# Kernel tuning notes

Measured on AMD Instinct MI355X. Metric: run time of the kernel, lower is better.

## Reference

```python
import jax, jax.numpy as jnp
import numpy as np

B, S, D, DQKV = 4, 2048, 1024, 1024

def setup_inputs() -> dict:
    key = jax.random.key(0)
    kx, kq, kk, kv = jax.random.split(key, 4)
    scale = 1.0 / np.sqrt(D)
    return {
        "x": jax.random.normal(kx, (B, S, D), dtype=jnp.float32),
        "wq": jax.random.normal(kq, (D, DQKV), dtype=jnp.float32) * scale,
        "wk": jax.random.normal(kk, (D, DQKV), dtype=jnp.float32) * scale,
        "wv": jax.random.normal(kv, (D, DQKV), dtype=jnp.float32) * scale,
    }

def reference(x, wq, wk, wv):
    # QKV projections: [B,S,D] @ [D,Dqkv] -> [B,S,Dqkv]
    q = jnp.einsum('bsd,de->bse', x, wq)
    k = jnp.einsum('bsd,de->bse', x, wk)
    v = jnp.einsum('bsd,de->bse', x, wv)
    # scores: [B,S,S], scaled by sqrt(dim_qkv)
    scores = jnp.einsum('bik,bjk->bij', q, k) / jnp.sqrt(jnp.asarray(DQKV, dtype=x.dtype))
    attn = jax.nn.softmax(scores, axis=-1)
    # output: [B,S,Dqkv]
    return jnp.einsum('bij,bjd->bid', attn, v)
```

## Files before the change

### kernel.cpp

```cpp
#include <hip/hip_runtime.h>
#include <cstdint>
#include <cstddef>

typedef __bf16 bf16;
typedef __bf16 bf16x4 __attribute__((ext_vector_type(4)));
typedef __bf16 bf16x8 __attribute__((ext_vector_type(8)));
typedef float  f32x4  __attribute__((ext_vector_type(4)));

#define BATCH 4
#define SEQ   2048
#define DIM   1024

__device__ __forceinline__ bf16 to_bf16(float f) {
    unsigned u = __builtin_bit_cast(unsigned, f);
    u += 0x7fffu + ((u >> 16) & 1u);
    unsigned short h = (unsigned short)(u >> 16);
    return __builtin_bit_cast(bf16, h);
}

__device__ __forceinline__ void load16_lds(const bf16* g, bf16* l) {
    __builtin_amdgcn_global_load_lds(
        (__attribute__((address_space(1))) void*)(g),
        (__attribute__((address_space(3))) void*)(l),
        16, 0, 0);
}

__device__ __forceinline__ void gemm_core64(
    const bf16* __restrict__ Abase, const bf16* __restrict__ Bbase,
    int K, int lda, int ldb, bf16* As, bf16* Bs, f32x4 acc[4][4])
{
    const int tid  = threadIdx.x;
    const int lane = tid & 63;
    const int wave = tid >> 6;
    const int wm   = (wave >> 1) * 64;
    const int wn   = (wave & 1) * 64;
    const int r16  = lane & 15;
    const int g    = lane >> 4;
    const int srow0 = wave * 8 + (lane >> 3);
    const int scoff = (((lane & 7) ^ ((lane >> 3) & 7)) * 8);
    const int ldsW  = wave * 512;

    for (int k0 = 0; k0 < K; k0 += 64) {
        __syncthreads();
#pragma unroll
        for (int j = 0; j < 4; ++j) {
            load16_lds(Abase + (size_t)(j * 32 + srow0) * lda + k0 + scoff,
                       As + j * 2048 + ldsW);
            load16_lds(Bbase + (size_t)(j * 32 + srow0) * ldb + k0 + scoff,
                       Bs + j * 2048 + ldsW);
        }
        __syncthreads();

#pragma unroll
        for (int h = 0; h < 2; ++h) {
            bf16x8 af[4], bfr[4];
            const int pc = h * 4 + g;
#pragma unroll
            for (int i = 0; i < 4; ++i) {
                const int p = pc ^ (r16 & 7);
                af[i]  = *(const bf16x8*)(As + (wm + i * 16 + r16) * 64 + p * 8);
                bfr[i] = *(const bf16x8*)(Bs + (wn + i * 16 + r16) * 64 + p * 8);
            }
#pragma unroll
            for (int mi = 0; mi < 4; ++mi)
#pragma unroll
                for (int ni = 0; ni < 4; ++ni)
                    acc[mi][ni] = __builtin_amdgcn_mfma_f32_16x16x32_bf16(
                        af[mi], bfr[ni], acc[mi][ni], 0, 0, 0);
        }
    }
}

__global__ __launch_bounds__(256, 4) void proj_gemm(
    const bf16* __restrict__ xb, const bf16* __restrict__ Wt,
    bf16* __restrict__ QK, bf16* __restrict__ Vt)
{
    __shared__ bf16 As[8192];
    __shared__ bf16 Bs[8192];
    f32x4 acc[4][4] = {};

    const int r = blockIdx.x;
    const bf16 *Ab, *Bb;
    bf16* Cb;
    int bx, byl;
    if (r < 1024) {
        const int c = r & 7, j = r >> 3;
        bx  = j & 15;
        byl = c + 8 * (j >> 4);
        Ab = xb + (size_t)byl * 128 * DIM;
        Bb = Wt + (size_t)bx * 128 * DIM;
        Cb = QK + (size_t)byl * 128 * 2048;
    } else {
        const int u = r - 1024;
        const int c = u & 7, j = u >> 3;
        bx = j & 15;
        const int p = c + 8 * (j >> 4);
        byl = p & 7;
        const int bz = p >> 3;
        Ab = Wt + (size_t)2 * DIM * DIM + (size_t)byl * 128 * DIM;
        Bb = xb + (size_t)bz * SEQ * DIM + (size_t)bx * 128 * DIM;
        Cb = Vt + (size_t)bz * DIM * SEQ + (size_t)byl * 128 * 2048;
    }
    gemm_core64(Ab, Bb, DIM, DIM, DIM, As, Bs, acc);

    const int lane = threadIdx.x & 63;
    const int wave = threadIdx.x >> 6;
    const int wm = (wave >> 1) * 64, wn = (wave & 1) * 64;
    const int rowO = wm + ((lane >> 4) * 4);
    const int colO = bx * 128 + wn + (lane & 15);
#pragma unroll
    for (int mi = 0; mi < 4; ++mi)
#pragma unroll
        for (int ni = 0; ni < 4; ++ni)
#pragma unroll
            for (int rr = 0; rr < 4; ++rr)
                Cb[(size_t)(rowO + mi * 16 + rr) * 2048 + colO + ni * 16] =
                    to_bf16(acc[mi][ni][rr]);
}

__global__ __launch_bounds__(256, 4) void gemm_scores(
    const bf16* __restrict__ A, const bf16* __restrict__ Bm, bf16* __restrict__ C,
    float* __restrict__ lsum)
{
    __shared__ bf16 As[8192];
    __shared__ bf16 Bs[8192];
    f32x4 acc[4][4] = {};

    const int d = blockIdx.x + 16 * (blockIdx.y + 16 * blockIdx.z);
    const int c = d & 7, j = d >> 3;
    const int bx = j & 15;
    const int p = c + 8 * (j >> 4);
    const int by = p & 15, bz = p >> 4;

    const int lda = 2 * DIM;
    const bf16* Ab = A  + (size_t)bz * SEQ * lda + (size_t)by * 128 * lda;
    const bf16* Bb = Bm + (size_t)bz * SEQ * lda + (size_t)bx * 128 * lda;
    bf16* Cb = C + (size_t)bz * SEQ * SEQ;
    gemm_core64(Ab, Bb, DIM, lda, lda, As, Bs, acc);

    const int lane = threadIdx.x & 63;
    const int wave = threadIdx.x >> 6;
    const int wm = (wave >> 1) * 64, wn = (wave & 1) * 64;
    const int rowBase = by * 128 + wm + ((lane >> 4) * 4);
    const int colBase = bx * 128 + wn + (lane & 15);

#pragma unroll
    for (int mi = 0; mi < 4; ++mi)
#pragma unroll
        for (int ni = 0; ni < 4; ++ni)
#pragma unroll
            for (int rr = 0; rr < 4; ++rr) {
                const float e = __expf(acc[mi][ni][rr] * 0.03125f);
                acc[mi][ni][rr] = e;
                Cb[(size_t)(rowBase + mi * 16 + rr) * SEQ + colBase + ni * 16] =
                    to_bf16(e);
            }

    float* ls = lsum + (size_t)bz * SEQ;
#pragma unroll
    for (int mi = 0; mi < 4; ++mi)
#pragma unroll
        for (int rr = 0; rr < 4; ++rr) {
            float s = acc[mi][0][rr] + acc[mi][1][rr] + acc[mi][2][rr] + acc[mi][3][rr];
            s += __shfl_xor(s, 1);
            s += __shfl_xor(s, 2);
            s += __shfl_xor(s, 4);
            s += __shfl_xor(s, 8);
            if ((lane & 15) == 0)
                atomicAdd(ls + rowBase + mi * 16 + rr, s);
        }
}

__global__ __launch_bounds__(256, 4) void gemm_pv(
    const bf16* __restrict__ A, const bf16* __restrict__ Bm, float* __restrict__ C,
    const float* __restrict__ lsum)
{
    __shared__ bf16 As[8192];
    __shared__ bf16 Bs[8192];
    f32x4 acc[4][4] = {};

    const int d = blockIdx.x + 8 * (blockIdx.y + 16 * blockIdx.z);
    const int c = d & 7, j = d >> 3;
    const int bx = j & 7;
    const int p = c + 8 * (j >> 3);
    const int by = p & 15, bz = p >> 4;

    const bf16* Ab = A  + (size_t)bz * SEQ * SEQ + (size_t)by * 128 * SEQ;
    const bf16* Bb = Bm + (size_t)bz * DIM * SEQ + (size_t)bx * 128 * SEQ;
    float* Cb = C + (size_t)bz * SEQ * DIM;
    gemm_core64(Ab, Bb, SEQ, SEQ, SEQ, As, Bs, acc);

    const int lane = threadIdx.x & 63;
    const int wave = threadIdx.x >> 6;
    const int wm = (wave >> 1) * 64, wn = (wave & 1) * 64;
    const int rowBase = by * 128 + wm + ((lane >> 4) * 4);
    const int colBase = bx * 128 + wn + (lane & 15);
    const float* ls = lsum + (size_t)bz * SEQ;
#pragma unroll
    for (int mi = 0; mi < 4; ++mi)
#pragma unroll
        for (int rr = 0; rr < 4; ++rr) {
            const float inv = __builtin_amdgcn_rcpf(ls[rowBase + mi * 16 + rr]);
#pragma unroll
            for (int ni = 0; ni < 4; ++ni)
                Cb[(size_t)(rowBase + mi * 16 + rr) * DIM + colBase + ni * 16] =
                    acc[mi][ni][rr] * inv;
        }
}

__global__ __launch_bounds__(256) void cvt_x(const float* __restrict__ x, bf16* __restrict__ y) {
    const size_t i = ((size_t)blockIdx.x * 256 + threadIdx.x) * 4;
    const float4 v = *(const float4*)(x + i);
    bf16x4 o = { to_bf16(v.x), to_bf16(v.y), to_bf16(v.z), to_bf16(v.w) };
    *(bf16x4*)(y + i) = o;
}

__global__ void cvt_w_t(const float* __restrict__ wq, const float* __restrict__ wk,
                        const float* __restrict__ wv, bf16* __restrict__ Wt)
{
    __shared__ float tile[32][33];
    const int sel = blockIdx.z;
    const float* w = (sel == 0) ? wq : (sel == 1) ? wk : wv;
    const int n0 = blockIdx.x * 32;
    const int k0 = blockIdx.y * 32;
    const int tx = threadIdx.x, ty = threadIdx.y;
#pragma unroll
    for (int j = 0; j < 32; j += 8)
        tile[ty + j][tx] = w[(size_t)(k0 + ty + j) * 1024 + n0 + tx];
    __syncthreads();
    bf16* dst = Wt + (size_t)sel * 1024 * 1024;
#pragma unroll
    for (int j = 0; j < 32; j += 8)
        dst[(size_t)(n0 + ty + j) * 1024 + k0 + tx] = to_bf16(tile[tx][ty + j]);
}

extern "C" void kernel_launch(void* const* d_in, const int* in_sizes, int n_in,
                              void* d_out, int out_size, void* d_ws, size_t ws_size,
                              hipStream_t stream)
{
    const float* x  = (const float*)d_in[0];
    const float* wq = (const float*)d_in[1];
    const float* wk = (const float*)d_in[2];
    const float* wv = (const float*)d_in[3];
    float* out = (float*)d_out;
    char* ws = (char*)d_ws;

    bf16*  xb   = (bf16*)(ws);
    bf16*  Wt   = (bf16*)(ws + (16u << 20));
    bf16*  QK   = (bf16*)(ws + (22u << 20));
    bf16*  Vt   = (bf16*)(ws + (54u << 20));
    bf16*  P    = (bf16*)(ws + (70u << 20));
    float* lsum = (float*)(ws + (102u << 20));

    hipMemsetAsync(lsum, 0, BATCH * SEQ * sizeof(float), stream);
    cvt_x<<<dim3(8192), dim3(256), 0, stream>>>(x, xb);
    cvt_w_t<<<dim3(32, 32, 3), dim3(32, 8), 0, stream>>>(wq, wk, wv, Wt);

    proj_gemm<<<dim3(1536), dim3(256), 0, stream>>>(xb, Wt, QK, Vt);

    gemm_scores<<<dim3(16, 16, 4), dim3(256), 0, stream>>>(QK, QK + DIM, P, lsum);

    gemm_pv<<<dim3(8, 16, 4), dim3(256), 0, stream>>>(P, Vt, out, lsum);
}
```

Measured before the change: 240.8 us.

## Halve PV tile height for more blocks and fuse prep kernels into one

Makes the shared GEMM core generic over the M tile height and runs the P·V GEMM with 64-row tiles, doubling its grid from 512 to 1024 blocks. With 256 CUs, 512 blocks is only two blocks per CU, so the change targets underfilled CUs and the tail, at the cost of re-reading Vt tiles more often and lower MFMA reuse per block. It also merges the memset, the x conversion and the weight transpose into one launch to cut per-launch overhead.

```diff
diff --git a/kernel.cpp b/kernel.cpp
--- a/kernel.cpp
+++ b/kernel.cpp
@@ -25,14 +25,16 @@
         16, 0, 0);
 }
 
+template<int BM>
 __device__ __forceinline__ void gemm_core64(
     const bf16* __restrict__ Abase, const bf16* __restrict__ Bbase,
-    int K, int lda, int ldb, bf16* As, bf16* Bs, f32x4 acc[4][4])
-{
+    int K, int lda, int ldb, bf16* As, bf16* Bs, f32x4 acc[BM / 32][4])
+{
+    constexpr int MI = BM / 32;
     const int tid  = threadIdx.x;
     const int lane = tid & 63;
     const int wave = tid >> 6;
-    const int wm   = (wave >> 1) * 64;
+    const int wm   = (wave >> 1) * (BM / 2);
     const int wn   = (wave & 1) * 64;
     const int r16  = lane & 15;
     const int g    = lane >> 4;
@@ -43,26 +45,27 @@
     for (int k0 = 0; k0 < K; k0 += 64) {
         __syncthreads();
 #pragma unroll
-        for (int j = 0; j < 4; ++j) {
+        for (int j = 0; j < BM / 32; ++j)
             load16_lds(Abase + (size_t)(j * 32 + srow0) * lda + k0 + scoff,
                        As + j * 2048 + ldsW);
+#pragma unroll
+        for (int j = 0; j < 4; ++j)
             load16_lds(Bbase + (size_t)(j * 32 + srow0) * ldb + k0 + scoff,
                        Bs + j * 2048 + ldsW);
-        }
         __syncthreads();
 
 #pragma unroll
         for (int h = 0; h < 2; ++h) {
-            bf16x8 af[4], bfr[4];
-            const int pc = h * 4 + g;
-#pragma unroll
-            for (int i = 0; i < 4; ++i) {
-                const int p = pc ^ (r16 & 7);
+            bf16x8 af[MI], bfr[4];
+            const int p = (h * 4 + g) ^ (r16 & 7);
+#pragma unroll
+            for (int i = 0; i < MI; ++i)
                 af[i]  = *(const bf16x8*)(As + (wm + i * 16 + r16) * 64 + p * 8);
+#pragma unroll
+            for (int i = 0; i < 4; ++i)
                 bfr[i] = *(const bf16x8*)(Bs + (wn + i * 16 + r16) * 64 + p * 8);
-            }
-#pragma unroll
-            for (int mi = 0; mi < 4; ++mi)
+#pragma unroll
+            for (int mi = 0; mi < MI; ++mi)
 #pragma unroll
                 for (int ni = 0; ni < 4; ++ni)
                     acc[mi][ni] = __builtin_amdgcn_mfma_f32_16x16x32_bf16(
@@ -101,7 +104,7 @@
         Bb = xb + (size_t)bz * SEQ * DIM + (size_t)bx * 128 * DIM;
         Cb = Vt + (size_t)bz * DIM * SEQ + (size_t)byl * 128 * 2048;
     }
-    gemm_core64(Ab, Bb, DIM, DIM, DIM, As, Bs, acc);
+    gemm_core64<128>(Ab, Bb, DIM, DIM, DIM, As, Bs, acc);
 
     const int lane = threadIdx.x & 63;
     const int wave = threadIdx.x >> 6;
@@ -136,7 +139,7 @@
     const bf16* Ab = A  + (size_t)bz * SEQ * lda + (size_t)by * 128 * lda;
     const bf16* Bb = Bm + (size_t)bz * SEQ * lda + (size_t)bx * 128 * lda;
     bf16* Cb = C + (size_t)bz * SEQ * SEQ;
-    gemm_core64(Ab, Bb, DIM, lda, lda, As, Bs, acc);
+    gemm_core64<128>(Ab, Bb, DIM, lda, lda, As, Bs, acc);
 
     const int lane = threadIdx.x & 63;
     const int wave = threadIdx.x >> 6;
@@ -175,29 +178,29 @@
     const bf16* __restrict__ A, const bf16* __restrict__ Bm, float* __restrict__ C,
     const float* __restrict__ lsum)
 {
-    __shared__ bf16 As[8192];
+    __shared__ bf16 As[4096];
     __shared__ bf16 Bs[8192];
-    f32x4 acc[4][4] = {};
-
-    const int d = blockIdx.x + 8 * (blockIdx.y + 16 * blockIdx.z);
+    f32x4 acc[2][4] = {};
+
+    const int d = blockIdx.x + 8 * (blockIdx.y + 32 * blockIdx.z);
     const int c = d & 7, j = d >> 3;
     const int bx = j & 7;
     const int p = c + 8 * (j >> 3);
-    const int by = p & 15, bz = p >> 4;
-
-    const bf16* Ab = A  + (size_t)bz * SEQ * SEQ + (size_t)by * 128 * SEQ;
+    const int by = p & 31, bz = p >> 5;
+
+    const bf16* Ab = A  + (size_t)bz * SEQ * SEQ + (size_t)by * 64 * SEQ;
     const bf16* Bb = Bm + (size_t)bz * DIM * SEQ + (size_t)bx * 128 * SEQ;
     float* Cb = C + (size_t)bz * SEQ * DIM;
-    gemm_core64(Ab, Bb, SEQ, SEQ, SEQ, As, Bs, acc);
+    gemm_core64<64>(Ab, Bb, SEQ, SEQ, SEQ, As, Bs, acc);
 
     const int lane = threadIdx.x & 63;
     const int wave = threadIdx.x >> 6;
-    const int wm = (wave >> 1) * 64, wn = (wave & 1) * 64;
-    const int rowBase = by * 128 + wm + ((lane >> 4) * 4);
+    const int wm = (wave >> 1) * 32, wn = (wave & 1) * 64;
+    const int rowBase = by * 64 + wm + ((lane >> 4) * 4);
     const int colBase = bx * 128 + wn + (lane & 15);
     const float* ls = lsum + (size_t)bz * SEQ;
 #pragma unroll
-    for (int mi = 0; mi < 4; ++mi)
+    for (int mi = 0; mi < 2; ++mi)
 #pragma unroll
         for (int rr = 0; rr < 4; ++rr) {
             const float inv = __builtin_amdgcn_rcpf(ls[rowBase + mi * 16 + rr]);
@@ -208,30 +211,39 @@
         }
 }
 
-__global__ __launch_bounds__(256) void cvt_x(const float* __restrict__ x, bf16* __restrict__ y) {
-    const size_t i = ((size_t)blockIdx.x * 256 + threadIdx.x) * 4;
-    const float4 v = *(const float4*)(x + i);
-    bf16x4 o = { to_bf16(v.x), to_bf16(v.y), to_bf16(v.z), to_bf16(v.w) };
-    *(bf16x4*)(y + i) = o;
-}
-
-__global__ void cvt_w_t(const float* __restrict__ wq, const float* __restrict__ wk,
-                        const float* __restrict__ wv, bf16* __restrict__ Wt)
+__global__ __launch_bounds__(256) void prep(
+    const float* __restrict__ x,  const float* __restrict__ wq,
+    const float* __restrict__ wk, const float* __restrict__ wv,
+    bf16* __restrict__ xb, bf16* __restrict__ Wt, float* __restrict__ lsum)
 {
     __shared__ float tile[32][33];
-    const int sel = blockIdx.z;
-    const float* w = (sel == 0) ? wq : (sel == 1) ? wk : wv;
-    const int n0 = blockIdx.x * 32;
-    const int k0 = blockIdx.y * 32;
-    const int tx = threadIdx.x, ty = threadIdx.y;
-#pragma unroll
-    for (int j = 0; j < 32; j += 8)
-        tile[ty + j][tx] = w[(size_t)(k0 + ty + j) * 1024 + n0 + tx];
-    __syncthreads();
-    bf16* dst = Wt + (size_t)sel * 1024 * 1024;
-#pragma unroll
-    for (int j = 0; j < 32; j += 8)
-        dst[(size_t)(n0 + ty + j) * 1024 + k0 + tx] = to_bf16(tile[tx][ty + j]);
+    const int b = blockIdx.x;
+    const int tid = threadIdx.x;
+    if (b < 8192) {
+        const size_t i = ((size_t)b * 256 + tid) * 4;
+        const float4 v = *(const float4*)(x + i);
+        bf16x4 o = { to_bf16(v.x), to_bf16(v.y), to_bf16(v.z), to_bf16(v.w) };
+        *(bf16x4*)(xb + i) = o;
+    } else if (b < 8192 + 3072) {
+        const int t   = b - 8192;
+        const int sel = t >> 10;
+        const int n0  = (t & 31) * 32;
+        const int k0  = ((t >> 5) & 31) * 32;
+        const float* w = (sel == 0) ? wq : (sel == 1) ? wk : wv;
+        const int tx = tid & 31, ty = tid >> 5;
+#pragma unroll
+        for (int j = 0; j < 32; j += 8)
+            tile[ty + j][tx] = w[(size_t)(k0 + ty + j) * 1024 + n0 + tx];
+        __syncthreads();
+        bf16* dst = Wt + (size_t)sel * 1024 * 1024;
+#pragma unroll
+        for (int j = 0; j < 32; j += 8)
+            dst[(size_t)(n0 + ty + j) * 1024 + k0 + tx] = to_bf16(tile[tx][ty + j]);
+    } else {
+#pragma unroll
+        for (int i = 0; i < 32; ++i)
+            lsum[i * 256 + tid] = 0.0f;
+    }
 }
 
 extern "C" void kernel_launch(void* const* d_in, const int* in_sizes, int n_in,
@@ -252,13 +264,12 @@
     bf16*  P    = (bf16*)(ws + (70u << 20));
     float* lsum = (float*)(ws + (102u << 20));
 
-    hipMemsetAsync(lsum, 0, BATCH * SEQ * sizeof(float), stream);
-    cvt_x<<<dim3(8192), dim3(256), 0, stream>>>(x, xb);
-    cvt_w_t<<<dim3(32, 32, 3), dim3(32, 8), 0, stream>>>(wq, wk, wv, Wt);
+    prep<<<dim3(8192 + 3072 + 1), dim3(256), 0, stream>>>(
+        x, wq, wk, wv, xb, Wt, lsum);
 
     proj_gemm<<<dim3(1536), dim3(256), 0, stream>>>(xb, Wt, QK, Vt);
 
     gemm_scores<<<dim3(16, 16, 4), dim3(256), 0, stream>>>(QK, QK + DIM, P, lsum);
 
-    gemm_pv<<<dim3(8, 16, 4), dim3(256), 0, stream>>>(P, Vt, out, lsum);
-}
+    gemm_pv<<<dim3(8, 32, 4), dim3(256), 0, stream>>>(P, Vt, out, lsum);
+}
```

Result: no change. 237.4 us (-1.4%).
